# Kernel optimization log

Measured on AMD Instinct MI355X. Metric: run time of the kernel, lower is better.

Reference implementation:

```python
import jax, jax.numpy as jnp
import numpy as np

H, DN, DR, DV = 16, 128, 64, 128   # heads, nope dim, rope dim, v dim
QR, KR = 1536, 512                 # q / kv lora ranks
HI, DI, TOPK = 32, 128, 512        # indexer heads, indexer head dim, index_topk

def rmsnorm(x, w, eps=1e-6):
    return x * jax.lax.rsqrt(jnp.mean(x * x, -1, keepdims=True) + eps) * w

def layernorm(x, w, b, eps=1e-5):
    m = jnp.mean(x, -1, keepdims=True)
    v = jnp.mean((x - m) ** 2, -1, keepdims=True)
    return (x - m) * jax.lax.rsqrt(v + eps) * w + b

def rope_interleaved(x, cos, sin):
    # x: [b,s,h,d]; cos,sin: [s,d//2]; pairs are (x[2j], x[2j+1])
    x0, x1 = x[..., 0::2], x[..., 1::2]
    c, s = cos[None, :, None, :], sin[None, :, None, :]
    return jnp.stack([x0 * c - x1 * s, x0 * s + x1 * c], -1).reshape(x.shape)

def rope_half(x, cos, sin):
    # non-interleaved variant: pairs are (x[j], x[j+d/2]); output = [real_half, imag_half]
    d = x.shape[-1] // 2
    x0, x1 = x[..., :d], x[..., d:]
    c, s = cos[None, :, None, :], sin[None, :, None, :]
    return jnp.concatenate([x0 * c - x1 * s, x0 * s + x1 * c], -1)

def setup_inputs():
    key = jax.random.key(0)
    B, S, DM = 1, 2048, 2048
    ks = jax.random.split(key, 10)
    w = lambda k, shape: jax.random.normal(k, shape, jnp.float32) * 0.02
    inp = {
        'hidden_states': jax.random.normal(ks[0], (B, S, DM), jnp.float32),
        'wq_a': w(ks[1], (QR, DM)),
        'q_norm_w': jnp.ones((QR,), jnp.float32),
        'wq_b': w(ks[2], (H * (DN + DR), QR)),
        'wkv_a': w(ks[3], (KR + DR, DM)),
        'kv_norm_w': jnp.ones((KR,), jnp.float32),
        'wkv_b': w(ks[4], (H * (DN + DV), KR)),
        'wo': w(ks[5], (DM, H * DV)),
        'idx_wq_b': w(ks[6], (HI * DI, QR)),
        'idx_wk': w(ks[7], (DI, DM)),
        'idx_kn_w': jnp.ones((DI,), jnp.float32),
        'idx_kn_b': jnp.zeros((DI,), jnp.float32),
        'idx_wproj': w(ks[8], (HI, DM)),
    }
    ang = jnp.arange(S, dtype=jnp.float32)[:, None] / (10000.0 ** (jnp.arange(0, DR, 2, dtype=jnp.float32) / DR))[None, :]
    inp['freqs_cos'], inp['freqs_sin'] = jnp.cos(ang), jnp.sin(ang)
    inp['mask'] = jnp.broadcast_to(
        jnp.where(jnp.tril(jnp.ones((S, S), bool)), 0.0, -jnp.inf).astype(jnp.float32), (B, S, S))
    return inp

def reference(hidden_states, freqs_cos, freqs_sin, mask, wq_a, q_norm_w, wq_b, wkv_a,
              kv_norm_w, wkv_b, wo, idx_wq_b, idx_wk, idx_kn_w, idx_kn_b, idx_wproj):
    B, S, DM = hidden_states.shape
    # --- MLA low-rank Q/KV projections ---
    qr = rmsnorm(hidden_states @ wq_a.T, q_norm_w)                       # [B,S,QR]
    q = (qr @ wq_b.T).reshape(B, S, H, DN + DR)
    q_pe = rope_interleaved(q[..., DN:], freqs_cos, freqs_sin)
    q = jnp.concatenate([q[..., :DN], q_pe], -1)                         # [B,S,H,192]
    kv_all = hidden_states @ wkv_a.T                                     # [B,S,KR+DR]
    kv = rmsnorm(kv_all[..., :KR], kv_norm_w)
    k_pe = rope_interleaved(kv_all[..., KR:][:, :, None, :], freqs_cos, freqs_sin)  # [B,S,1,DR]
    kvp = (kv @ wkv_b.T).reshape(B, S, H, DN + DV)
    k = jnp.concatenate([kvp[..., :DN], jnp.broadcast_to(k_pe, (B, S, H, DR))], -1)
    v = kvp[..., DN:]                                                    # [B,S,H,DV]
    scores = jnp.einsum('bshd,bthd->bsht', q, k) * (DN + DR) ** -0.5
    # --- indexer: relu-weighted scores -> top-k token set ---
    qi = (qr @ idx_wq_b.T).reshape(B, S, HI, DI)
    qi = jnp.concatenate([rope_half(qi[..., :DR], freqs_cos, freqs_sin), qi[..., DR:]], -1)
    ki = layernorm(hidden_states @ idx_wk.T, idx_kn_w, idx_kn_b)         # [B,S,DI]
    ki_pe = rope_half(ki[..., :DR][:, :, None, :], freqs_cos, freqs_sin)[:, :, 0, :]
    ki = jnp.concatenate([ki_pe, ki[..., DR:]], -1)
    wts = (hidden_states @ idx_wproj.T) * HI ** -0.5                     # [B,S,HI]
    iscores = jax.nn.relu(jnp.einsum('bshd,btd->bsht', qi, ki) * DI ** -0.5) * wts[..., None]
    index_scores = iscores.sum(2) + mask                                 # [B,S,S]
    topk_idx = jax.lax.top_k(index_scores, TOPK)[1]                      # [B,S,TOPK]
    index_mask = jnp.full((B, S, S), -jnp.inf, jnp.float32)
    index_mask = index_mask.at[jnp.arange(B)[:, None, None],
                               jnp.arange(S)[None, :, None], topk_idx].set(0.0)
    # --- sparse-masked attention ---
    scores = scores + (index_mask + mask)[:, :, None, :]
    probs = jax.nn.softmax(scores, axis=-1)
    out = jnp.einsum('bsht,bthd->bshd', probs, v).reshape(B, S, H * DV)
    return out @ wo.T
```

## Files before the change

### kernel.cpp

```cpp
#include <hip/hip_runtime.h>
#include <stdint.h>

typedef unsigned int uint;
typedef unsigned short u16;
typedef unsigned long long u64;

typedef float  f32x4 __attribute__((ext_vector_type(4)));
typedef uint   u32x4 __attribute__((ext_vector_type(4)));
typedef u16    u16x4 __attribute__((ext_vector_type(4)));
typedef u16    u16x8 __attribute__((ext_vector_type(8)));
typedef __bf16 bf16x8 __attribute__((ext_vector_type(8)));

#define DEV static __device__ __forceinline__
#define MFMA(a,b,c) __builtin_amdgcn_mfma_f32_16x16x32_bf16((a),(b),(c),0,0,0)
#define GLDS(src,dst) __builtin_amdgcn_global_load_lds((const __attribute__((address_space(1))) void*)(src),(__attribute__((address_space(3))) void*)(dst),16,0,0)

DEV u16 f2bf(float x){ union{float f;uint u;} v; v.f=x; return (u16)((v.u + 0x7fffu + ((v.u>>16)&1u))>>16); }
DEV float bf2f(u16 b){ union{uint u;float f;} v; v.u=((uint)b)<<16; return v.f; }
DEV int imin(int a,int b){ return a<b?a:b; }

__global__ void cvt_all(
    const float* __restrict__ hs, const float* __restrict__ wqa, const float* __restrict__ iwqb,
    const float* __restrict__ iwk, const float* __restrict__ iwp,
    const float* __restrict__ wqbw, const float* __restrict__ wkva, const float* __restrict__ wkvb,
    const float* __restrict__ wow,
    u16* __restrict__ hid_hi, u16* __restrict__ hid_lo, u16* __restrict__ wqa_hi, u16* __restrict__ wqa_lo,
    u16* __restrict__ iwqb_hi, u16* __restrict__ iwqb_lo, u16* __restrict__ kiwp_hi, u16* __restrict__ kiwp_lo,
    u16* __restrict__ wqb_b, u16* __restrict__ wkva_b, u16* __restrict__ wkvb_b, u16* __restrict__ wo_b)
{
  int i = blockIdx.x*blockDim.x + threadIdx.x;
  int st = gridDim.x*blockDim.x;
  for(; i < 6537216; i += st){
    const float* src; u16 *dh, *dl=nullptr; int j; bool split;
    if(i < 1048576){ src=hs;   dh=hid_hi;  dl=hid_lo;  j=i;         split=true; }
    else if(i < 1835008){ src=wqa;  dh=wqa_hi;  dl=wqa_lo;  j=i-1048576; split=true; }
    else if(i < 3407872){ src=iwqb; dh=iwqb_hi; dl=iwqb_lo; j=i-1835008; split=true; }
    else if(i < 3473408){ src=iwk;  dh=kiwp_hi; dl=kiwp_lo; j=i-3407872; split=true; }
    else if(i < 3489792){ src=iwp;  dh=kiwp_hi+128*2048; dl=kiwp_lo+128*2048; j=i-3473408; split=true; }
    else if(i < 4669440){ src=wqbw; dh=wqb_b;  j=i-3489792; split=false; }
    else if(i < 4964352){ src=wkva; dh=wkva_b; j=i-4669440; split=false; }
    else if(i < 5488640){ src=wkvb; dh=wkvb_b; j=i-4964352; split=false; }
    else               { src=wow;  dh=wo_b;   j=i-5488640; split=false; }
    f32x4 x = reinterpret_cast<const f32x4*>(src)[j];
    u16x4 h;
    #pragma unroll
    for(int k=0;k<4;k++) h[k]=f2bf(x[k]);
    reinterpret_cast<u16x4*>(dh)[j]=h;
    if(split){
      u16x4 l;
      #pragma unroll
      for(int k=0;k<4;k++) l[k]=f2bf(x[k]-bf2f(h[k]));
      reinterpret_cast<u16x4*>(dl)[j]=l;
    }
  }
}

DEV void stage128x32(const u16* __restrict__ gbase, int ld, int row0, int maxrow, int k0, u16* lds){
  int tid = threadIdx.x, w = tid>>6, l = tid&63;
  #pragma unroll
  for(int j=0;j<2;j++){
    int seg = w + j*4;
    int row = seg*16 + (l>>2);
    int gr = row0 + row; if(gr > maxrow) gr = maxrow;
    const u16* g = gbase + (size_t)gr*ld + k0 + (l&3)*8;
    GLDS(g, lds + seg*512);
  }
}

template<int SPLIT>
__global__ __launch_bounds__(256,2) void gemm_glds(
    const u16* __restrict__ Ah, const u16* __restrict__ Al, int lda,
    const u16* __restrict__ Bh, const u16* __restrict__ Bl, int ldb,
    float* __restrict__ C, int ldc, int M, int N, int K)
{
  __shared__ u16 sAh[128*32];
  __shared__ u16 sBh[128*32];
  __shared__ u16 sAl[SPLIT?128*32:8];
  __shared__ u16 sBl[SPLIT?128*32:8];
  const int tid = threadIdx.x;
  const int w = tid>>6, l = tid&63;
  const int wr = w>>1, wc = w&1;
  const int l15 = l&15, l16 = l>>4;

  int gx = gridDim.x;
  int nwg = gx*gridDim.y;
  int orig = blockIdx.x + gx*blockIdx.y;
  int qq = nwg>>3, rr = nwg&7, xc = orig&7, oo = orig>>3;
  int wg = (xc<rr ? xc*(qq+1) : rr*(qq+1)+(xc-rr)*qq) + oo;
  int m0 = (wg/gx)*128, n0 = (wg%gx)*128;

  int kz = K/(int)gridDim.z;
  int kbeg = blockIdx.z*kz;

  f32x4 acc[4][4];
  #pragma unroll
  for(int m=0;m<4;m++)
    #pragma unroll
    for(int n=0;n<4;n++) acc[m][n] = f32x4{0.f,0.f,0.f,0.f};

  for(int k0=kbeg; k0<kbeg+kz; k0+=32){
    __syncthreads();
    stage128x32(Ah, lda, m0, M-1, k0, sAh);
    stage128x32(Bh, ldb, n0, N-1, k0, sBh);
    if(SPLIT){
      stage128x32(Al, lda, m0, M-1, k0, sAl);
      stage128x32(Bl, ldb, n0, N-1, k0, sBl);
    }
    asm volatile("s_waitcnt vmcnt(0)" ::: "memory");
    __syncthreads();
    bf16x8 ah[4], bh[4];
    #pragma unroll
    for(int m=0;m<4;m++) ah[m] = *reinterpret_cast<const bf16x8*>(&sAh[(wr*64+m*16+l15)*32 + l16*8]);
    #pragma unroll
    for(int n=0;n<4;n++) bh[n] = *reinterpret_cast<const bf16x8*>(&sBh[(wc*64+n*16+l15)*32 + l16*8]);
    #pragma unroll
    for(int m=0;m<4;m++)
      #pragma unroll
      for(int n=0;n<4;n++) acc[m][n] = MFMA(ah[m], bh[n], acc[m][n]);
    if(SPLIT){
      bf16x8 t[4];
      #pragma unroll
      for(int n=0;n<4;n++) t[n] = *reinterpret_cast<const bf16x8*>(&sBl[(wc*64+n*16+l15)*32 + l16*8]);
      #pragma unroll
      for(int m=0;m<4;m++)
        #pragma unroll
        for(int n=0;n<4;n++) acc[m][n] = MFMA(ah[m], t[n], acc[m][n]);
      #pragma unroll
      for(int m=0;m<4;m++) t[m] = *reinterpret_cast<const bf16x8*>(&sAl[(wr*64+m*16+l15)*32 + l16*8]);
      #pragma unroll
      for(int m=0;m<4;m++)
        #pragma unroll
        for(int n=0;n<4;n++) acc[m][n] = MFMA(t[m], bh[n], acc[m][n]);
    }
  }
  float* Cp = C + (size_t)blockIdx.z*M*ldc;
  #pragma unroll
  for(int m=0;m<4;m++){
    int row = m0 + wr*64 + m*16 + l16*4;
    #pragma unroll
    for(int n=0;n<4;n++){
      int col = n0 + wc*64 + n*16 + l15;
      if(col < N){
        #pragma unroll
        for(int r=0;r<4;r++){
          int rrow = row + r;
          if(rrow < M) Cp[(size_t)rrow*ldc + col] = acc[m][n][r];
        }
      }
    }
  }
}

__global__ __launch_bounds__(256) void rmsnorm_qr_split(
    const float* __restrict__ in, const float* __restrict__ w,
    u16* __restrict__ hi, u16* __restrict__ lo)
{
  int s = blockIdx.x, tid = threadIdx.x;
  __shared__ float red[4];
  const float* x = in + (size_t)s*1536;
  const size_t plane = 2048ull*1536;
  float xv[6]; float ss=0.f;
  #pragma unroll
  for(int i=0;i<6;i++){ int c = tid+i*256; xv[i] = x[c] + x[plane+c]; ss += xv[i]*xv[i]; }
  #pragma unroll
  for(int o=32;o>0;o>>=1) ss += __shfl_down(ss,o,64);
  if((tid&63)==0) red[tid>>6]=ss;
  __syncthreads();
  float total = red[0]+red[1]+red[2]+red[3];
  float scale = rsqrtf(total*(1.0f/1536.0f) + 1e-6f);
  #pragma unroll
  for(int i=0;i<6;i++){
    int c = tid + i*256;
    float vv = xv[i]*scale*w[c];
    u16 hv = f2bf(vv);
    hi[(size_t)s*1536+c]=hv;
    lo[(size_t)s*1536+c]=f2bf(vv - bf2f(hv));
  }
}

__global__ __launch_bounds__(256) void kv_norm_rope(
    const float* __restrict__ kva, const float* __restrict__ w,
    const float* __restrict__ fcos, const float* __restrict__ fsin,
    u16* __restrict__ kvb, float* __restrict__ kpe)
{
  int s = blockIdx.x, tid = threadIdx.x;
  __shared__ float red[4];
  const size_t plane = 2048ull*576;
  float xv[2]={0.f,0.f};
  #pragma unroll
  for(int c=0;c<4;c++){
    const float* xp = kva + (size_t)c*plane + (size_t)s*576;
    xv[0]+=xp[tid]; xv[1]+=xp[tid+256];
  }
  float ss = xv[0]*xv[0]+xv[1]*xv[1];
  #pragma unroll
  for(int o=32;o>0;o>>=1) ss += __shfl_down(ss,o,64);
  if((tid&63)==0) red[tid>>6]=ss;
  __syncthreads();
  float total = red[0]+red[1]+red[2]+red[3];
  float scale = rsqrtf(total*(1.0f/512.0f)+1e-6f);
  #pragma unroll
  for(int i=0;i<2;i++){ int c=tid+i*256; kvb[(size_t)s*512+c]=f2bf(xv[i]*scale*w[c]); }
  if(tid<32){
    float x0=0.f, x1=0.f;
    #pragma unroll
    for(int c=0;c<4;c++){
      const float* xp = kva + (size_t)c*plane + (size_t)s*576;
      x0 += xp[512+2*tid]; x1 += xp[513+2*tid];
    }
    float c0=fcos[(size_t)s*32+tid], s_=fsin[(size_t)s*32+tid];
    kpe[(size_t)s*64+2*tid]   = x0*c0 - x1*s_;
    kpe[(size_t)s*64+2*tid+1] = x0*s_ + x1*c0;
  }
}

__global__ __launch_bounds__(256) void rope_q_cvt(const float* __restrict__ qpre,
    const float* __restrict__ fcos, const float* __restrict__ fsin, u16* __restrict__ qb)
{
  int s = blockIdx.x;
  const float* rowp = qpre + (size_t)s*3072;
  u16* op = qb + (size_t)s*3072;
  for(int idx=threadIdx.x; idx<3072; idx+=256){
    int hh = idx/192, d = idx - hh*192;
    float vv;
    if(d < 128) vv = rowp[hh*192 + d];
    else{
      int i2 = (d-128)>>1;
      float c0 = fcos[(size_t)s*32+i2], s_ = fsin[(size_t)s*32+i2];
      float x0 = rowp[hh*192 + 128 + 2*i2], x1 = rowp[hh*192 + 129 + 2*i2];
      vv = ((d&1)==0) ? (x0*c0 - x1*s_) : (x0*s_ + x1*c0);
    }
    op[idx] = f2bf(vv);
  }
}

__global__ __launch_bounds__(256) void qi_rope_split(const float* __restrict__ qpre,
    const float* __restrict__ fcos, const float* __restrict__ fsin,
    u16* __restrict__ hi, u16* __restrict__ lo)
{
  int s = blockIdx.x;
  const float* rowp = qpre + (size_t)s*4096;
  for(int idx=threadIdx.x; idx<4096; idx+=256){
    int hh = idx>>7, d = idx&127;
    const float* hb = rowp + (hh<<7);
    float vv;
    if(d<32){ float c0=fcos[(size_t)s*32+d], s_=fsin[(size_t)s*32+d]; vv = hb[d]*c0 - hb[d+32]*s_; }
    else if(d<64){ int i2=d-32; float c0=fcos[(size_t)s*32+i2], s_=fsin[(size_t)s*32+i2]; vv = hb[i2]*s_ + hb[d]*c0; }
    else vv = hb[d];
    u16 hv = f2bf(vv);
    hi[(size_t)s*4096+idx]=hv;
    lo[(size_t)s*4096+idx]=f2bf(vv - bf2f(hv));
  }
}

__global__ __launch_bounds__(128) void ki_ln_rope_split(
    const float* __restrict__ kpre, const float* __restrict__ w, const float* __restrict__ bb,
    const float* __restrict__ fcos, const float* __restrict__ fsin,
    u16* __restrict__ hi, u16* __restrict__ lo, float* __restrict__ wts_out)
{
  int s = blockIdx.x, tid = threadIdx.x;
  __shared__ float red[2];
  __shared__ float ybuf[128];
  const size_t plane = 2048ull*160;
  float x = 0.f;
  #pragma unroll
  for(int c=0;c<8;c++) x += kpre[(size_t)c*plane + (size_t)s*160 + tid];
  if(tid<32){
    float ws = 0.f;
    #pragma unroll
    for(int c=0;c<8;c++) ws += kpre[(size_t)c*plane + (size_t)s*160 + 128 + tid];
    wts_out[(size_t)s*160 + 128 + tid] = ws;
  }
  float v = x;
  #pragma unroll
  for(int o=32;o>0;o>>=1) v += __shfl_down(v,o,64);
  if((tid&63)==0) red[tid>>6]=v;
  __syncthreads();
  float mean = (red[0]+red[1])*(1.f/128.f);
  __syncthreads();
  float dx = x - mean;
  v = dx*dx;
  #pragma unroll
  for(int o=32;o>0;o>>=1) v += __shfl_down(v,o,64);
  if((tid&63)==0) red[tid>>6]=v;
  __syncthreads();
  float var = (red[0]+red[1])*(1.f/128.f);
  float y = dx*rsqrtf(var+1e-5f)*w[tid] + bb[tid];
  ybuf[tid]=y;
  __syncthreads();
  float r;
  if(tid<32){ float c0=fcos[(size_t)s*32+tid], s_=fsin[(size_t)s*32+tid]; r = ybuf[tid]*c0 - ybuf[tid+32]*s_; }
  else if(tid<64){ int i2=tid-32; float c0=fcos[(size_t)s*32+i2], s_=fsin[(size_t)s*32+i2]; r = ybuf[i2]*s_ + ybuf[tid]*c0; }
  else r = y;
  u16 hv=f2bf(r);
  hi[(size_t)s*128+tid]=hv;
  lo[(size_t)s*128+tid]=f2bf(r-bf2f(hv));
}

__global__ __launch_bounds__(256) void transpose_assemble(const float* __restrict__ kvp,
    const float* __restrict__ kpe, u16* __restrict__ vt, u16* __restrict__ kb){
  __shared__ u16 T[64*136];
  int s0 = blockIdx.x*64, h = blockIdx.y;
  int tid = threadIdx.x;
  for(int idx=tid; idx<64*192; idx+=256){
    int r = idx/192, d = idx - r*192;
    float val = (d<128) ? kvp[(size_t)(s0+r)*4096 + h*256 + d] : kpe[(size_t)(s0+r)*64 + (d-128)];
    kb[((size_t)(s0+r)*16 + h)*192 + d] = f2bf(val);
  }
  #pragma unroll
  for(int i=0;i<8;i++){
    int ch = i*256 + tid;
    int r = ch>>5, cc = ch&31;
    f32x4 x = *reinterpret_cast<const f32x4*>(&kvp[(size_t)(s0+r)*4096 + h*256 + 128 + cc*4]);
    u16x4 y;
    #pragma unroll
    for(int j=0;j<4;j++) y[j] = f2bf(x[j]);
    *reinterpret_cast<u16x4*>(&T[r*136 + cc*4]) = y;
  }
  __syncthreads();
  #pragma unroll
  for(int i=0;i<4;i++){
    int ch = i*256 + tid;
    int d = ch>>3, sc = ch&7;
    u16x8 y;
    #pragma unroll
    for(int j=0;j<8;j++) y[j] = T[(sc*8+j)*136 + d];
    *reinterpret_cast<u16x8*>(&vt[((size_t)h*128 + d)*2048 + s0 + sc*8]) = y;
  }
}

DEV void isc_pass128(const u16* __restrict__ Q, const u16* __restrict__ Kb,
                     f32x4 (&sc)[4][2], int wm, int wn, int l15, int l16){
  #pragma unroll
  for(int ks=0;ks<4;ks++){
    bf16x8 a[4], b[2];
    #pragma unroll
    for(int m=0;m<4;m++){
      int row = wm*64 + m*16 + l15;
      a[m] = *reinterpret_cast<const bf16x8*>(&Q[row*128 + ((((ks<<2)+l16) ^ (row&7))<<3)]);
    }
    #pragma unroll
    for(int n=0;n<2;n++){
      int row = wn*32 + n*16 + l15;
      b[n] = *reinterpret_cast<const bf16x8*>(&Kb[row*128 + ((((ks<<2)+l16) ^ (row&7))<<3)]);
    }
    #pragma unroll
    for(int m=0;m<4;m++)
      #pragma unroll
      for(int n=0;n<2;n++) sc[m][n] = MFMA(a[m], b[n], sc[m][n]);
  }
}

__global__ __launch_bounds__(512,2) void idx_scores6(
    const u16* __restrict__ qih, const u16* __restrict__ qil,
    const u16* __restrict__ kih, const u16* __restrict__ kil,
    const float* __restrict__ wts,
    float* __restrict__ p0, float* __restrict__ p1, float* __restrict__ p2, float* __restrict__ p3)
{
  __shared__ u16 Kh[128*128];
  __shared__ u16 Kl[128*128];
  __shared__ u16 Qb[2][128*128];
  int orig = blockIdx.x;
  int bid = (orig&7)*68 + (orig>>3);
  int tileIdx = bid>>2, hg = bid&3;
  int si=0, t=tileIdx;
  while(t >= si+1){ t -= si+1; si++; }
  int s0 = si*128, t0 = t*128;
  float* plane = (hg==0)?p0:(hg==1)?p1:(hg==2)?p2:p3;
  float* outp = plane + (size_t)tileIdx*16384;
  int h0 = hg*8;
  int tid=threadIdx.x, w=tid>>6, l=tid&63;
  int wm=w>>2, wn=w&3, l15=l&15, l16=l>>4;
  #pragma unroll
  for(int rnd=0;rnd<4;rnd++){
    int cid = rnd*512 + w*64 + l;
    int row = cid>>4, cc = cid&15;
    int scc = cc ^ (row&7);
    GLDS(kih + (size_t)(t0+row)*128 + scc*8, Kh + rnd*4096 + w*512);
    GLDS(kil + (size_t)(t0+row)*128 + scc*8, Kl + rnd*4096 + w*512);
  }
  #pragma unroll
  for(int rnd=0;rnd<4;rnd++){
    int cid = rnd*512 + w*64 + l;
    int row = cid>>4, cc = cid&15;
    int scc = cc ^ (row&7);
    GLDS(qih + (size_t)(s0+row)*4096 + h0*128 + scc*8, Qb[0] + rnd*4096 + w*512);
  }
  asm volatile("s_waitcnt vmcnt(0)" ::: "memory");
  __syncthreads();
  f32x4 accI[4][2], sc[4][2];
  #pragma unroll
  for(int m=0;m<4;m++) for(int n=0;n<2;n++) accI[m][n] = f32x4{0.f,0.f,0.f,0.f};
  const float cscale = 0.015625f;
  for(int s=0;s<16;s++){
    int nxt = s+1;
    if(nxt < 16){
      const u16* src = (nxt&1) ? qil : qih;
      int hh = h0 + (nxt>>1);
      u16* dst = Qb[nxt&1];
      #pragma unroll
      for(int rnd=0;rnd<4;rnd++){
        int cid = rnd*512 + w*64 + l;
        int row = cid>>4, cc = cid&15;
        int scc = cc ^ (row&7);
        GLDS(src + (size_t)(s0+row)*4096 + hh*128 + scc*8, dst + rnd*4096 + w*512);
      }
    }
    const u16* Q = Qb[s&1];
    if((s&1)==0){
      #pragma unroll
      for(int m=0;m<4;m++) for(int n=0;n<2;n++) sc[m][n] = f32x4{0.f,0.f,0.f,0.f};
      isc_pass128(Q, Kh, sc, wm, wn, l15, l16);
      isc_pass128(Q, Kl, sc, wm, wn, l15, l16);
    } else {
      isc_pass128(Q, Kh, sc, wm, wn, l15, l16);
      int hh = h0 + (s>>1);
      #pragma unroll
      for(int m=0;m<4;m++)
        #pragma unroll
        for(int r=0;r<4;r++){
          float wv = wts[(size_t)(s0+wm*64+m*16+l16*4+r)*160 + 128 + hh]*cscale;
          #pragma unroll
          for(int n=0;n<2;n++) accI[m][n][r] += fmaxf(sc[m][n][r],0.f)*wv;
        }
    }
    asm volatile("s_waitcnt vmcnt(0)" ::: "memory");
    __syncthreads();
  }
  #pragma unroll
  for(int m=0;m<4;m++)
    #pragma unroll
    for(int n=0;n<2;n++)
      #pragma unroll
      for(int r=0;r<4;r++)
        outp[(wm*64+m*16+l16*4+r)*128 + wn*32 + n*16 + l15] = accI[m][n][r];
}

DEV uint fkey(float f){ union{float f;uint u;} v; v.f=f; return (v.u & 0x80000000u) ? ~v.u : (v.u | 0x80000000u); }

__global__ __launch_bounds__(256) void topk_mask(
    const float* __restrict__ p0, const float* __restrict__ p1,
    const float* __restrict__ p2, const float* __restrict__ p3, u64* __restrict__ bits)
{
  int s = blockIdx.x;
  int n = s+1;
  int tid = threadIdx.x;
  if(n <= 512){
    for(int wI=tid; wI<32; wI+=256){
      u64 m=0; int base=wI*64;
      if(base < n){ int cnt=n-base; m = (cnt>=64)? ~0ull : ((1ull<<cnt)-1ull); }
      bits[(size_t)s*32+wI]=m;
    }
    return;
  }
  __shared__ float row[2048];
  __shared__ uint hist[256];
  __shared__ uint sh_B, sh_k;
  __shared__ uint wcnt[32];
  int si = s>>7, sr = s&127;
  size_t triBase = (size_t)(si*(si+1)/2);
  for(int c=tid; c<n; c+=256){
    size_t off = (triBase + (size_t)(c>>7))*16384 + (size_t)sr*128 + (c&127);
    row[c] = p0[off]+p1[off]+p2[off]+p3[off];
  }
  __syncthreads();
  uint prefix=0, k=512;
  for(int shift=24; shift>=0; shift-=8){
    hist[tid]=0;
    __syncthreads();
    for(int t2=tid;t2<n;t2+=256){
      uint u = fkey(row[t2]);
      bool ok = (shift==24) || ((u>>(shift+8)) == (prefix>>(shift+8)));
      if(ok) atomicAdd(&hist[(u>>shift)&255u],1u);
    }
    __syncthreads();
    if(tid==0){
      uint c=0;
      for(int b2=255;b2>=0;b2--){
        c += hist[b2];
        if(c>=k){ sh_B=(uint)b2; sh_k = k-(c-hist[b2]); break; }
      }
    }
    __syncthreads();
    prefix |= sh_B<<shift;
    k = sh_k;
    __syncthreads();
  }
  uint thr = prefix;
  if(tid<32) wcnt[tid]=0;
  __syncthreads();
  int nw = (n+63)>>6;
  if(tid < nw){
    int base=tid*64, end = base+64; if(end>n) end=n;
    uint c=0;
    for(int t2=base;t2<end;t2++) if(fkey(row[t2])==thr) c++;
    wcnt[tid]=c;
  }
  __syncthreads();
  if(tid==0){
    uint runv=0;
    for(int i=0;i<32;i++){ uint c=wcnt[i]; wcnt[i]=runv; runv+=c; }
  }
  __syncthreads();
  if(tid<32){
    u64 m=0; int base=tid*64;
    if(base<n){
      uint rank = wcnt[tid];
      int end = base+64; if(end>n) end=n;
      for(int t2=base;t2<end;t2++){
        uint u = fkey(row[t2]);
        if(u>thr) m |= (1ull<<(t2-base));
        else if(u==thr){ if(rank<k) m |= (1ull<<(t2-base)); rank++; }
      }
    }
    bits[(size_t)s*32+tid]=m;
  }
}

__global__ __launch_bounds__(256,3) void flash_attn(
    const u16* __restrict__ q, const u16* __restrict__ k, const u16* __restrict__ vt,
    const u64* __restrict__ bits, u16* __restrict__ o,
    u16* __restrict__ Opart, float* __restrict__ ml)
{
  __shared__ u16 Ks[64*192];
  __shared__ u16 Vt[128*64];
  __shared__ u16 Pl[64*72];
  int h = blockIdx.y;
  int pp = blockIdx.x;
  int sblk=0, chunk=0;
  for(int i=0;i<32;i++){
    int sb = 31-i; int ncc = (sb>>3)+1;
    if(pp < ncc){ sblk=sb; chunk=pp; break; }
    pp -= ncc;
  }
  int nc = (sblk>>3)+1, ntiles = sblk+1, s0 = sblk*64;
  int tid=threadIdx.x, w=tid>>6, l=tid&63;
  int l15=l&15, l16=l>>4;
  const float sscale = 0.07216878364870323f;
  bf16x8 qf[6];
  #pragma unroll
  for(int ks=0;ks<6;ks++)
    qf[ks] = *reinterpret_cast<const bf16x8*>(&q[((size_t)(s0+w*16+l15)*16 + h)*192 + ks*32 + l16*8]);
  f32x4 Oa[8];
  #pragma unroll
  for(int n=0;n<8;n++) Oa[n] = f32x4{0.f,0.f,0.f,0.f};
  float mrun[4], lrun[4];
  #pragma unroll
  for(int r=0;r<4;r++){ mrun[r]=-__builtin_inff(); lrun[r]=0.f; }
  int tt0 = chunk*8, tt1 = imin(tt0+8, ntiles);
  for(int tt=tt0; tt<tt1; tt++){
    int t0 = tt*64;
    __syncthreads();
    #pragma unroll
    for(int rnd=0;rnd<6;rnd++){
      int cid = rnd*256 + w*64 + l;
      int row = cid/24, cc = cid - row*24;
      int scc = cc ^ (row&7);
      GLDS(k + ((size_t)(t0+row)*16 + h)*192 + scc*8, Ks + rnd*2048 + w*512);
    }
    #pragma unroll
    for(int rnd=0;rnd<4;rnd++){
      int cid = rnd*256 + w*64 + l;
      int row = cid>>3, cc = cid&7;
      int scc = cc ^ (row&7);
      GLDS(vt + ((size_t)h*128 + row)*2048 + t0 + scc*8, Vt + rnd*2048 + w*512);
    }
    asm volatile("s_waitcnt vmcnt(0)" ::: "memory");
    __syncthreads();
    f32x4 S[4];
    #pragma unroll
    for(int n=0;n<4;n++) S[n] = f32x4{0.f,0.f,0.f,0.f};
    #pragma unroll
    for(int ks=0;ks<6;ks++){
      bf16x8 b[4];
      #pragma unroll
      for(int n=0;n<4;n++){
        int row = n*16+l15;
        b[n] = *reinterpret_cast<const bf16x8*>(&Ks[row*192 + ((((ks<<2)+l16) ^ (row&7))<<3)]);
      }
      #pragma unroll
      for(int n=0;n<4;n++) S[n] = MFMA(qf[ks], b[n], S[n]);
    }
    #pragma unroll
    for(int r=0;r<4;r++){
      int srow = s0 + w*16 + l16*4 + r;
      u64 wrd = bits[(size_t)srow*32 + (t0>>6)];
      float mx = -__builtin_inff();
      #pragma unroll
      for(int n=0;n<4;n++){
        int bitp = n*16 + l15;
        int tcol = t0 + bitp;
        bool ok = (tcol <= srow) && ((wrd>>bitp)&1ull);
        float val = ok ? S[n][r]*sscale : -__builtin_inff();
        S[n][r] = val;
        mx = fmaxf(mx, val);
      }
      #pragma unroll
      for(int off=1;off<16;off<<=1) mx = fmaxf(mx, __shfl_xor(mx, off, 64));
      float mold = mrun[r];
      float mnew = fmaxf(mold, mx);
      bool inf0 = (mnew == -__builtin_inff());
      float alpha = inf0 ? 1.f : __expf(mold - mnew);
      float rs = 0.f;
      #pragma unroll
      for(int n=0;n<4;n++){
        float p = inf0 ? 0.f : __expf(S[n][r] - mnew);
        S[n][r] = p;
        rs += p;
      }
      #pragma unroll
      for(int off=1;off<16;off<<=1) rs += __shfl_xor(rs, off, 64);
      mrun[r]=mnew;
      lrun[r] = lrun[r]*alpha + rs;
      #pragma unroll
      for(int n=0;n<8;n++) Oa[n][r] *= alpha;
    }
    #pragma unroll
    for(int n=0;n<4;n++)
      #pragma unroll
      for(int r=0;r<4;r++)
        Pl[(w*16+l16*4+r)*72 + n*16+l15] = f2bf(S[n][r]);
    #pragma unroll
    for(int ks=0;ks<2;ks++){
      bf16x8 a = *reinterpret_cast<const bf16x8*>(&Pl[(w*16+l15)*72 + ks*32 + l16*8]);
      bf16x8 bb[8];
      #pragma unroll
      for(int n=0;n<8;n++){
        int d = n*16+l15;
        bb[n] = *reinterpret_cast<const bf16x8*>(&Vt[d*64 + ((((ks<<2)+l16) ^ (d&7))<<3)]);
      }
      #pragma unroll
      for(int n=0;n<8;n++) Oa[n] = MFMA(a, bb[n], Oa[n]);
    }
  }
  if(nc == 1){
    #pragma unroll
    for(int r=0;r<4;r++){
      int srow = s0 + w*16 + l16*4 + r;
      float inv = 1.f/lrun[r];
      #pragma unroll
      for(int n=0;n<8;n++)
        o[(size_t)srow*2048 + h*128 + n*16 + l15] = f2bf(Oa[n][r]*inv);
    }
  } else {
    int part = ((h*32 + sblk)<<2) + chunk;
    u16* Op = Opart + (size_t)part*8192;
    #pragma unroll
    for(int r=0;r<4;r++){
      int rit = w*16 + l16*4 + r;
      #pragma unroll
      for(int n=0;n<8;n++)
        Op[rit*128 + n*16 + l15] = f2bf(Oa[n][r]);
      if(l15==0){
        ml[(size_t)part*128 + rit*2]   = mrun[r];
        ml[(size_t)part*128 + rit*2+1] = lrun[r];
      }
    }
  }
}

__global__ __launch_bounds__(256) void flash_combine(
    const u16* __restrict__ Opart, const float* __restrict__ ml, u16* __restrict__ o)
{
  int b = blockIdx.x;
  int h = b/24, sblk = 8 + (b%24);
  int nc = (sblk>>3)+1;
  int tid = threadIdx.x;
  int r = tid>>2, dq = (tid&3)*32;
  int s0 = sblk*64;
  int pbase = (h*32+sblk)<<2;
  float m[4], lv[4], wgt[4];
  float M = -__builtin_inff();
  for(int c=0;c<nc;c++){
    m[c]  = ml[(size_t)(pbase+c)*128 + r*2];
    lv[c] = ml[(size_t)(pbase+c)*128 + r*2 + 1];
    if(lv[c] > 0.f) M = fmaxf(M, m[c]);
  }
  float L = 0.f;
  for(int c=0;c<nc;c++){
    wgt[c] = (lv[c] > 0.f) ? __expf(m[c]-M) : 0.f;
    L += lv[c]*wgt[c];
  }
  float inv = 1.f/L;
  for(int dd=0; dd<32; dd+=8){
    float accv[8];
    #pragma unroll
    for(int j=0;j<8;j++) accv[j]=0.f;
    for(int c=0;c<nc;c++){
      u16x8 pv = *reinterpret_cast<const u16x8*>(&Opart[(size_t)(pbase+c)*8192 + r*128 + dq + dd]);
      #pragma unroll
      for(int j=0;j<8;j++) accv[j] += wgt[c]*bf2f(pv[j]);
    }
    u16x8 ov;
    #pragma unroll
    for(int j=0;j<8;j++) ov[j] = f2bf(accv[j]*inv);
    *reinterpret_cast<u16x8*>(&o[(size_t)(s0+r)*2048 + h*128 + dq + dd]) = ov;
  }
}

extern "C" void kernel_launch(void* const* d_in, const int* in_sizes, int n_in,
                              void* d_out, int out_size, void* d_ws, size_t ws_size,
                              hipStream_t stream)
{
  (void)in_sizes; (void)n_in; (void)out_size;
  const float* hs   = (const float*)d_in[0];
  const float* wqa  = (const float*)d_in[1];
  const float* qnw  = (const float*)d_in[2];
  const float* wqbw = (const float*)d_in[3];
  const float* wkva = (const float*)d_in[4];
  const float* kvnw = (const float*)d_in[5];
  const float* wkvb = (const float*)d_in[6];
  const float* wow  = (const float*)d_in[7];
  const float* iwqb = (const float*)d_in[8];
  const float* iwk  = (const float*)d_in[9];
  const float* iknw = (const float*)d_in[10];
  const float* iknb = (const float*)d_in[11];
  const float* iwp  = (const float*)d_in[12];
  const float* fcos = (const float*)d_in[13];
  const float* fsin = (const float*)d_in[14];
  float* outp = (float*)d_out;

  char* base = (char*)d_ws;
  size_t off = 0;
  auto alloc = [&](size_t bytes)->char*{ char* p = base+off; off += (bytes+255)&~(size_t)255; return p; };
  u16* hid_hi = (u16*)alloc(2048ull*2048*2);
  u16* hid_lo = (u16*)alloc(2048ull*2048*2);
  u16* wqa_hi = (u16*)alloc(1536ull*2048*2);
  u16* wqa_lo = (u16*)alloc(1536ull*2048*2);
  u16* wqb_b  = (u16*)alloc(3072ull*1536*2);
  u16* wkva_b = (u16*)alloc(576ull*2048*2);
  u16* wkvb_b = (u16*)alloc(4096ull*512*2);
  u16* wo_b   = (u16*)alloc(2048ull*2048*2);
  u16* iwqb_hi= (u16*)alloc(4096ull*1536*2);
  u16* iwqb_lo= (u16*)alloc(4096ull*1536*2);
  u16* kiwp_hi= (u16*)alloc(160ull*2048*2);
  u16* kiwp_lo= (u16*)alloc(160ull*2048*2);
  float* kiwp_C=(float*)alloc(2048ull*160*4);
  u16* qr_hi  = (u16*)alloc(2048ull*1536*2);
  u16* qr_lo  = (u16*)alloc(2048ull*1536*2);
  u16* kv_b   = (u16*)alloc(2048ull*512*2);
  float* kpe  = (float*)alloc(2048ull*64*4);
  u16* k_b    = (u16*)alloc(2048ull*16*192*2);
  u16* v_t    = (u16*)alloc(16ull*128*2048*2);
  u16* ki_hi  = (u16*)alloc(2048ull*128*2);
  u16* ki_lo  = (u16*)alloc(2048ull*128*2);
  u64* bits   = (u64*)alloc(2048ull*32*8);
  u16* attn_b = (u16*)alloc(2048ull*2048*2);
  float* reg1 = (float*)alloc(2048ull*4096*4);
  if(ws_size < off) return;

  u16* q_b      = wqa_hi;
  u16* qi_hi    = hid_hi;
  u16* qi_lo    = iwqb_hi;
  float* ml     = (float*)qr_lo;
  float* qr_pre = reg1;
  float* q_pre  = reg1;
  float* kva_part = reg1;
  float* kvp    = reg1;
  float* kiwp_part = reg1;
  float* qi_pre = reg1;
  const size_t PLANE = 136ull*16384;
  float* ip0 = reg1;
  float* ip1 = reg1 + PLANE;
  float* ip2 = reg1 + 2*PLANE;
  float* ip3 = (float*)wqb_b;
  u16* Opart = (u16*)reg1;

  auto G1 = [&](const u16* A,int lda,const u16* B,int ldb,float* C,int ldc,int M,int N,int K,int z){
    dim3 g((unsigned)((N+127)/128), (unsigned)((M+127)/128), (unsigned)z);
    gemm_glds<0><<<g,256,0,stream>>>(A,nullptr,lda,B,nullptr,ldb,C,ldc,M,N,K);
  };
  auto G3 = [&](const u16* Ah,const u16* Al,int lda,const u16* Bh,const u16* Bl,int ldb,float* C,int ldc,int M,int N,int K,int z){
    dim3 g((unsigned)((N+127)/128), (unsigned)((M+127)/128), (unsigned)z);
    gemm_glds<1><<<g,256,0,stream>>>(Ah,Al,lda,Bh,Bl,ldb,C,ldc,M,N,K);
  };

  cvt_all<<<2048,256,0,stream>>>(hs,wqa,iwqb,iwk,iwp,wqbw,wkva,wkvb,wow,
      hid_hi,hid_lo,wqa_hi,wqa_lo,iwqb_hi,iwqb_lo,kiwp_hi,kiwp_lo,
      wqb_b,wkva_b,wkvb_b,wo_b);

  G3(hid_hi,hid_lo,2048, wqa_hi,wqa_lo,2048, qr_pre,1536, 2048,1536,2048, 2);
  rmsnorm_qr_split<<<2048,256,0,stream>>>(qr_pre, qnw, qr_hi, qr_lo);

  G1(qr_hi,1536, wqb_b,1536, q_pre,3072, 2048,3072,1536, 1);
  rope_q_cvt<<<2048,256,0,stream>>>(q_pre, fcos, fsin, q_b);

  G1(hid_hi,2048, wkva_b,2048, kva_part,576, 2048,576,2048, 4);
  kv_norm_rope<<<2048,256,0,stream>>>(kva_part, kvnw, fcos, fsin, kv_b, kpe);
  G1(kv_b,512, wkvb_b,512, kvp,4096, 2048,4096,512, 1);
  transpose_assemble<<<dim3(32,16),256,0,stream>>>(kvp, kpe, v_t, k_b);

  G3(hid_hi,hid_lo,2048, kiwp_hi,kiwp_lo,2048, kiwp_part,160, 2048,160,2048, 8);
  ki_ln_rope_split<<<2048,128,0,stream>>>(kiwp_part, iknw, iknb, fcos, fsin, ki_hi, ki_lo, kiwp_C);

  G3(qr_hi,qr_lo,1536, iwqb_hi,iwqb_lo,1536, qi_pre,4096, 2048,4096,1536, 1);
  qi_rope_split<<<2048,256,0,stream>>>(qi_pre, fcos, fsin, qi_hi, qi_lo);

  idx_scores6<<<544,512,0,stream>>>(qi_hi, qi_lo, ki_hi, ki_lo, kiwp_C, ip0, ip1, ip2, ip3);
  topk_mask<<<2048,256,0,stream>>>(ip0, ip1, ip2, ip3, bits);

  flash_attn<<<dim3(80,16),256,0,stream>>>(q_b, k_b, v_t, bits, attn_b, Opart, ml);
  flash_combine<<<384,256,0,stream>>>(Opart, ml, attn_b);
  G1(attn_b,2048, wo_b,2048, outp,2048, 2048,2048,2048, 1);
}
```

Before: 587.2 us.

## Deepen GEMM K-tile, cache indexer weights in LDS, parallelize top-k bucket scan

The single-precision bf16 GEMM path now uses a K tile of 64 instead of 32, halving the number of barrier and wait rounds per K loop at the cost of more LDS. The indexer score kernel preloads the per-row head weights into a padded LDS table once, instead of reading them from global memory on every head iteration. The top-k radix select replaces the serial single-thread bucket scan with a parallel suffix-sum across 256 threads, which adds extra barriers.

```diff
diff --git a/kernel.cpp b/kernel.cpp
--- a/kernel.cpp
+++ b/kernel.cpp
@@ -55,28 +55,38 @@
   }
 }
 
-DEV void stage128x32(const u16* __restrict__ gbase, int ld, int row0, int maxrow, int k0, u16* lds){
+template<int BK>
+DEV void stageT(const u16* __restrict__ gbase, int ld, int row0, int maxrow, int k0, u16* lds){
   int tid = threadIdx.x, w = tid>>6, l = tid&63;
-  #pragma unroll
-  for(int j=0;j<2;j++){
-    int seg = w + j*4;
-    int row = seg*16 + (l>>2);
-    int gr = row0 + row; if(gr > maxrow) gr = maxrow;
-    const u16* g = gbase + (size_t)gr*ld + k0 + (l&3)*8;
-    GLDS(g, lds + seg*512);
-  }
-}
-
-template<int SPLIT>
+  if(BK==32){
+    #pragma unroll
+    for(int j=0;j<2;j++){
+      int seg = w + j*4;
+      int row = seg*16 + (l>>2);
+      int gr = row0 + row; if(gr > maxrow) gr = maxrow;
+      GLDS(gbase + (size_t)gr*ld + k0 + (l&3)*8, lds + seg*512);
+    }
+  } else {
+    #pragma unroll
+    for(int j=0;j<4;j++){
+      int c = w + j*4;
+      int row = c*8 + (l>>3);
+      int gr = row0 + row; if(gr > maxrow) gr = maxrow;
+      GLDS(gbase + (size_t)gr*ld + k0 + (l&7)*8, lds + c*512);
+    }
+  }
+}
+
+template<int SPLIT, int BK>
 __global__ __launch_bounds__(256,2) void gemm_glds(
     const u16* __restrict__ Ah, const u16* __restrict__ Al, int lda,
     const u16* __restrict__ Bh, const u16* __restrict__ Bl, int ldb,
     float* __restrict__ C, int ldc, int M, int N, int K)
 {
-  __shared__ u16 sAh[128*32];
-  __shared__ u16 sBh[128*32];
-  __shared__ u16 sAl[SPLIT?128*32:8];
-  __shared__ u16 sBl[SPLIT?128*32:8];
+  __shared__ u16 sAh[128*BK];
+  __shared__ u16 sBh[128*BK];
+  __shared__ u16 sAl[SPLIT?128*BK:8];
+  __shared__ u16 sBl[SPLIT?128*BK:8];
   const int tid = threadIdx.x;
   const int w = tid>>6, l = tid&63;
   const int wr = w>>1, wc = w&1;
@@ -98,39 +108,42 @@
     #pragma unroll
     for(int n=0;n<4;n++) acc[m][n] = f32x4{0.f,0.f,0.f,0.f};
 
-  for(int k0=kbeg; k0<kbeg+kz; k0+=32){
+  for(int k0=kbeg; k0<kbeg+kz; k0+=BK){
     __syncthreads();
-    stage128x32(Ah, lda, m0, M-1, k0, sAh);
-    stage128x32(Bh, ldb, n0, N-1, k0, sBh);
+    stageT<BK>(Ah, lda, m0, M-1, k0, sAh);
+    stageT<BK>(Bh, ldb, n0, N-1, k0, sBh);
     if(SPLIT){
-      stage128x32(Al, lda, m0, M-1, k0, sAl);
-      stage128x32(Bl, ldb, n0, N-1, k0, sBl);
+      stageT<BK>(Al, lda, m0, M-1, k0, sAl);
+      stageT<BK>(Bl, ldb, n0, N-1, k0, sBl);
     }
     asm volatile("s_waitcnt vmcnt(0)" ::: "memory");
     __syncthreads();
-    bf16x8 ah[4], bh[4];
-    #pragma unroll
-    for(int m=0;m<4;m++) ah[m] = *reinterpret_cast<const bf16x8*>(&sAh[(wr*64+m*16+l15)*32 + l16*8]);
-    #pragma unroll
-    for(int n=0;n<4;n++) bh[n] = *reinterpret_cast<const bf16x8*>(&sBh[(wc*64+n*16+l15)*32 + l16*8]);
-    #pragma unroll
-    for(int m=0;m<4;m++)
-      #pragma unroll
-      for(int n=0;n<4;n++) acc[m][n] = MFMA(ah[m], bh[n], acc[m][n]);
-    if(SPLIT){
-      bf16x8 t[4];
-      #pragma unroll
-      for(int n=0;n<4;n++) t[n] = *reinterpret_cast<const bf16x8*>(&sBl[(wc*64+n*16+l15)*32 + l16*8]);
+    #pragma unroll
+    for(int kk=0;kk<BK/32;kk++){
+      bf16x8 ah[4], bh[4];
+      #pragma unroll
+      for(int m=0;m<4;m++) ah[m] = *reinterpret_cast<const bf16x8*>(&sAh[(wr*64+m*16+l15)*BK + kk*32 + l16*8]);
+      #pragma unroll
+      for(int n=0;n<4;n++) bh[n] = *reinterpret_cast<const bf16x8*>(&sBh[(wc*64+n*16+l15)*BK + kk*32 + l16*8]);
       #pragma unroll
       for(int m=0;m<4;m++)
         #pragma unroll
-        for(int n=0;n<4;n++) acc[m][n] = MFMA(ah[m], t[n], acc[m][n]);
-      #pragma unroll
-      for(int m=0;m<4;m++) t[m] = *reinterpret_cast<const bf16x8*>(&sAl[(wr*64+m*16+l15)*32 + l16*8]);
-      #pragma unroll
-      for(int m=0;m<4;m++)
+        for(int n=0;n<4;n++) acc[m][n] = MFMA(ah[m], bh[n], acc[m][n]);
+      if(SPLIT){
+        bf16x8 t[4];
         #pragma unroll
-        for(int n=0;n<4;n++) acc[m][n] = MFMA(t[m], bh[n], acc[m][n]);
+        for(int n=0;n<4;n++) t[n] = *reinterpret_cast<const bf16x8*>(&sBl[(wc*64+n*16+l15)*BK + kk*32 + l16*8]);
+        #pragma unroll
+        for(int m=0;m<4;m++)
+          #pragma unroll
+          for(int n=0;n<4;n++) acc[m][n] = MFMA(ah[m], t[n], acc[m][n]);
+        #pragma unroll
+        for(int m=0;m<4;m++) t[m] = *reinterpret_cast<const bf16x8*>(&sAl[(wr*64+m*16+l15)*BK + kk*32 + l16*8]);
+        #pragma unroll
+        for(int m=0;m<4;m++)
+          #pragma unroll
+          for(int n=0;n<4;n++) acc[m][n] = MFMA(t[m], bh[n], acc[m][n]);
+      }
     }
   }
   float* Cp = C + (size_t)blockIdx.z*M*ldc;
@@ -360,6 +373,7 @@
   __shared__ u16 Kh[128*128];
   __shared__ u16 Kl[128*128];
   __shared__ u16 Qb[2][128*128];
+  __shared__ float Wl[128*9];
   int orig = blockIdx.x;
   int bid = (orig&7)*68 + (orig>>3);
   int tileIdx = bid>>2, hg = bid&3;
@@ -371,6 +385,7 @@
   int h0 = hg*8;
   int tid=threadIdx.x, w=tid>>6, l=tid&63;
   int wm=w>>2, wn=w&3, l15=l&15, l16=l>>4;
+  const float cscale = 0.015625f;
   #pragma unroll
   for(int rnd=0;rnd<4;rnd++){
     int cid = rnd*512 + w*64 + l;
@@ -386,12 +401,17 @@
     int scc = cc ^ (row&7);
     GLDS(qih + (size_t)(s0+row)*4096 + h0*128 + scc*8, Qb[0] + rnd*4096 + w*512);
   }
+  #pragma unroll
+  for(int it=0;it<2;it++){
+    int idx = it*512 + tid;
+    int row = idx>>3, hh = idx&7;
+    Wl[row*9+hh] = wts[(size_t)(s0+row)*160 + 128 + h0 + hh]*cscale;
+  }
   asm volatile("s_waitcnt vmcnt(0)" ::: "memory");
   __syncthreads();
   f32x4 accI[4][2], sc[4][2];
   #pragma unroll
   for(int m=0;m<4;m++) for(int n=0;n<2;n++) accI[m][n] = f32x4{0.f,0.f,0.f,0.f};
-  const float cscale = 0.015625f;
   for(int s=0;s<16;s++){
     int nxt = s+1;
     if(nxt < 16){
@@ -414,12 +434,12 @@
       isc_pass128(Q, Kl, sc, wm, wn, l15, l16);
     } else {
       isc_pass128(Q, Kh, sc, wm, wn, l15, l16);
-      int hh = h0 + (s>>1);
+      int hh = s>>1;
       #pragma unroll
       for(int m=0;m<4;m++)
         #pragma unroll
         for(int r=0;r<4;r++){
-          float wv = wts[(size_t)(s0+wm*64+m*16+l16*4+r)*160 + 128 + hh]*cscale;
+          float wv = Wl[(wm*64+m*16+l16*4+r)*9 + hh];
           #pragma unroll
           for(int n=0;n<2;n++) accI[m][n][r] += fmaxf(sc[m][n][r],0.f)*wv;
         }
@@ -474,13 +494,14 @@
       if(ok) atomicAdd(&hist[(u>>shift)&255u],1u);
     }
     __syncthreads();
-    if(tid==0){
-      uint c=0;
-      for(int b2=255;b2>=0;b2--){
-        c += hist[b2];
-        if(c>=k){ sh_B=(uint)b2; sh_k = k-(c-hist[b2]); break; }
-      }
-    }
+    for(int offd=1; offd<256; offd<<=1){
+      uint add = (tid+offd<256)? hist[tid+offd] : 0u;
+      __syncthreads();
+      hist[tid] += add;
+      __syncthreads();
+    }
+    uint nxtv = (tid<255)? hist[tid+1] : 0u;
+    if(hist[tid]>=k && nxtv<k){ sh_B=(uint)tid; sh_k = k - nxtv; }
     __syncthreads();
     prefix |= sh_B<<shift;
     k = sh_k;
@@ -768,11 +789,11 @@
 
   auto G1 = [&](const u16* A,int lda,const u16* B,int ldb,float* C,int ldc,int M,int N,int K,int z){
     dim3 g((unsigned)((N+127)/128), (unsigned)((M+127)/128), (unsigned)z);
-    gemm_glds<0><<<g,256,0,stream>>>(A,nullptr,lda,B,nullptr,ldb,C,ldc,M,N,K);
+    gemm_glds<0,64><<<g,256,0,stream>>>(A,nullptr,lda,B,nullptr,ldb,C,ldc,M,N,K);
   };
   auto G3 = [&](const u16* Ah,const u16* Al,int lda,const u16* Bh,const u16* Bl,int ldb,float* C,int ldc,int M,int N,int K,int z){
     dim3 g((unsigned)((N+127)/128), (unsigned)((M+127)/128), (unsigned)z);
-    gemm_glds<1><<<g,256,0,stream>>>(Ah,Al,lda,Bh,Bl,ldb,C,ldc,M,N,K);
+    gemm_glds<1,32><<<g,256,0,stream>>>(Ah,Al,lda,Bh,Bl,ldb,C,ldc,M,N,K);
   };
 
   cvt_all<<<2048,256,0,stream>>>(hs,wqa,iwqb,iwk,iwp,wqbw,wkva,wkvb,wow,
```

Measured after the change: 554.6 us. 5.6% less time.
